# Kernel tuning notes

Hardware: AMD Instinct MI355X
Metric: run time of the kernel (lower is better)

Reference implementation:

```python
import jax, jax.numpy as jnp
import numpy as np

DIM = 2048          # SDR dimension
CTX = 512           # top-down context (grid code) dimension
B = 8192            # batch of independent samples
N_PV = DIM // 4     # 512 PV interneurons
N_SV = DIM // 8     # 256 SOM/VIP interneurons
ALPHA_POS = 1.0 / 10.0   # dt / tau_pos
ALPHA_NEG = 1.0 / 10.0   # dt / tau_neg


def setup_inputs() -> dict:
    key = jax.random.key(0)
    ks = jax.random.split(key, 14)
    sc = 1.0 / np.sqrt(DIM)
    sc_sv = 1.0 / np.sqrt(N_SV)
    xav = np.sqrt(6.0 / (CTX + DIM))  # xavier uniform bound for predictor
    u = lambda k, shp, s: jax.random.uniform(k, shp, dtype=jnp.float32) * s
    return {
        "x_batch": jax.random.uniform(ks[0], (B, DIM), dtype=jnp.float32),
        "context_batch": jax.random.normal(ks[1], (B, CTX), dtype=jnp.float32),
        "r_pos_batch": jax.random.uniform(ks[2], (B, DIM), dtype=jnp.float32),
        "r_neg_batch": jax.random.uniform(ks[3], (B, DIM), dtype=jnp.float32),
        "W_pred": jax.random.uniform(ks[4], (DIM, CTX), jnp.float32, -xav, xav),
        "b_pred": jnp.zeros((DIM,), jnp.float32),
        "W_pv1_ff": u(ks[5], (N_PV, DIM), sc),
        "W_pv2_td": u(ks[6], (N_PV, DIM), sc),
        "W_vip_td": u(ks[7], (N_SV, DIM), sc),
        "W_som_in": u(ks[8], (N_SV, DIM), sc),
        "W_vip_som": u(ks[9], (N_SV, N_SV), sc_sv),
        "W_inh_pe_pos": u(ks[10], (DIM, N_PV), sc),
        "W_inh_pe_neg": u(ks[11], (DIM, N_PV), sc),
        "W_som_dend": u(ks[12], (DIM, N_SV), sc),
    }


def reference(x_batch, context_batch, r_pos_batch, r_neg_batch,
              W_pred, b_pred, W_pv1_ff, W_pv2_td, W_vip_td, W_som_in,
              W_vip_som, W_inh_pe_pos, W_inh_pe_neg, W_som_dend):
    relu = jax.nn.relu
    # top-down prediction: (B, CTX) @ (CTX, DIM) -> (B, DIM)
    predicted = context_batch @ W_pred.T + b_pred
    # interneuron circuit (Nemati 2025)
    r_pv1 = relu(x_batch @ W_pv1_ff.T)                               # (B, N_PV)
    r_pv2 = relu(predicted @ W_pv2_td.T)                             # (B, N_PV)
    r_vip = relu(predicted @ W_vip_td.T)                             # (B, N_SV)
    r_som = relu(relu(x_batch @ W_som_in.T) - r_vip @ W_vip_som.T)   # (B, N_SV)
    # signed prediction errors with somatic/dendritic inhibition
    pe_pos = relu(x_batch - predicted - r_pv2 @ W_inh_pe_pos.T)
    pe_neg = relu(predicted - x_batch - r_pv1 @ W_inh_pe_neg.T - r_som @ W_som_dend.T)
    # low-pass temporal filter of PE states
    new_r_pos = (1.0 - ALPHA_POS) * r_pos_batch + ALPHA_POS * pe_pos
    new_r_neg = (1.0 - ALPHA_NEG) * r_neg_batch + ALPHA_NEG * pe_neg
    return (new_r_pos, new_r_neg)
```

## Files before the change

kernel.cpp:

```cpp
#include <hip/hip_runtime.h>
#include <hip/hip_bf16.h>
#include <stdint.h>
#include <stddef.h>

#define DIMV 2048
#define CTXV 512
#define BV   8192
#define NPV  512
#define NSV  256

typedef __attribute__((ext_vector_type(8))) __bf16 bf16x8;
typedef __attribute__((ext_vector_type(4))) __bf16 bf16x4;
typedef __attribute__((ext_vector_type(4))) float f32x4;

__device__ __forceinline__ size_t fmq(int base_r, int Cb, int lhi, int llo, int nks) {
    const int kc = (Cb >> 3) + (lhi >> 1);
    return ((size_t)(base_r >> 4) * nks + (kc >> 2)) * 64 + (size_t)(kc & 3) * 16 + llo;
}

struct FmJob { const float* src; char* dst; int lognks; int ld; int trans; };
struct FmArgs { FmJob j[12]; unsigned cum[13]; };

__global__ __launch_bounds__(256) void cvt_fm(FmArgs a) {
    const unsigned total = a.cum[12];
    for (unsigned c = blockIdx.x * blockDim.x + threadIdx.x; c < total;
         c += gridDim.x * blockDim.x) {
        int seg = 0;
#pragma unroll
        for (int t = 1; t < 12; ++t) seg = (c >= a.cum[t]) ? t : seg;
        const FmJob jb = a.j[seg];
        const unsigned q = c - a.cum[seg];
        const int llo = q & 15, ch = (q >> 4) & 3;
        const unsigned blk = q >> 6;
        const unsigned s = blk & ((1u << jb.lognks) - 1u);
        const unsigned g = blk >> jb.lognks;
        const int row = g * 16 + llo;
        const int k0  = s * 32 + ch * 8;
        bf16x8 o;
        if (!jb.trans) {
            f32x4 v0 = *(const f32x4*)(jb.src + (size_t)row * jb.ld + k0);
            f32x4 v1 = *(const f32x4*)(jb.src + (size_t)row * jb.ld + k0 + 4);
#pragma unroll
            for (int e = 0; e < 4; ++e) { o[e] = (__bf16)v0[e]; o[e + 4] = (__bf16)v1[e]; }
        } else {
#pragma unroll
            for (int e = 0; e < 8; ++e)
                o[e] = (__bf16)jb.src[(size_t)(k0 + e) * jb.ld + row];
        }
        *(bf16x8*)(jb.dst + (size_t)q * 16) = o;
    }
}

__global__ __launch_bounds__(512)
void bias_comb(const float* __restrict__ Wpv2, const float* __restrict__ Wvip,
               const float* __restrict__ b, float* __restrict__ out) {
    const int tid  = threadIdx.x;
    const int gw   = blockIdx.x * 8 + (tid >> 6);
    const int lane = tid & 63;
    const float* row = (gw < 512) ? (Wpv2 + (size_t)gw * 2048)
                                  : (Wvip + (size_t)(gw - 512) * 2048);
    float acc = 0.f;
#pragma unroll
    for (int c = 0; c < 8; ++c) {
        const int j = lane * 32 + c * 4;
        f32x4 w  = *(const f32x4*)(row + j);
        f32x4 bb = *(const f32x4*)(b + j);
#pragma unroll
        for (int e = 0; e < 4; ++e) acc += w[e] * bb[e];
    }
#pragma unroll
    for (int off = 32; off > 0; off >>= 1) acc += __shfl_down(acc, off);
    if (lane == 0) out[gw] = acc;
}

#define GEOM4                                                     \
    const int tid  = threadIdx.x;                                 \
    const int wave = tid >> 6;                                    \
    const int lane = tid & 63;                                    \
    const int lhi  = lane >> 4;                                   \
    const int llo  = lane & 15;                                   \
    const int wr   = wave >> 1;                                   \
    const int wc   = wave & 1;

#define SETPA(Abase, nksA_)                                                   \
    _Pragma("unroll")                                                         \
    for (int i_ = 0; i_ < 2; ++i_) {                                          \
        const int g_ = (m0 + wr * 32 + i_ * 16) >> 4;                         \
        pa[i_] = (const char*)(Abase) + ((size_t)g_ * (nksA_)) * 1024 + lane * 16; \
    }
#define SETPW(Wbase, nksW_, nbase)                                            \
    _Pragma("unroll")                                                         \
    for (int j_ = 0; j_ < 4; ++j_) {                                          \
        const int g_ = ((nbase) + wc * 64 + j_ * 16) >> 4;                    \
        pw[j_] = (const char*)(Wbase) + ((size_t)g_ * (nksW_)) * 1024 + lane * 16; \
    }
#define LD6(AF, BF, OFS)                                                      \
    _Pragma("unroll")                                                         \
    for (int i_ = 0; i_ < 2; ++i_) AF[i_] = *(const bf16x8*)(pa[i_] + (OFS)); \
    _Pragma("unroll")                                                         \
    for (int j_ = 0; j_ < 4; ++j_) BF[j_] = *(const bf16x8*)(pw[j_] + (OFS));
#define ADV2                                                                  \
    _Pragma("unroll")                                                         \
    for (int i_ = 0; i_ < 2; ++i_) pa[i_] += 2048;                            \
    _Pragma("unroll")                                                         \
    for (int j_ = 0; j_ < 4; ++j_) pw[j_] += 2048;
#define MFMA8(af, bfr, acc)                                                   \
    __builtin_amdgcn_s_setprio(1);                                            \
    _Pragma("unroll")                                                         \
    for (int i = 0; i < 2; ++i)                                               \
        _Pragma("unroll")                                                     \
        for (int j = 0; j < 4; ++j)                                           \
            acc[i][j] = __builtin_amdgcn_mfma_f32_16x16x32_bf16(bfr[j], af[i], acc[i][j], 0, 0, 0); \
    __builtin_amdgcn_s_setprio(0);

struct GemmDesc {
    const char* A; int nksA;
    const char* W1; const char* W2; int nksW;
    int NB1, ntN, nsteps, epi;
    const float* bias;
    const char* subp; int nksSub;
    char* out1; int nksO1; char* out2; int nksO2;
};

__global__ __launch_bounds__(256, 3)
void pe_gemm7(GemmDesc dA_, GemmDesc dB_, GemmDesc dC_, int s1, int s2)
{
    const int nwg = gridDim.x;
    const int bid = blockIdx.x;
    int wg = (bid & 7) * (nwg >> 3) + (bid >> 3);
    GemmDesc d = dA_;
    if (wg >= s2)      { d = dC_; wg -= s2; }
    else if (wg >= s1) { d = dB_; wg -= s1; }
    if (d.out1 == nullptr) return;

    const int bx = wg / d.ntN;
    const int by = wg - bx * d.ntN;
    const int m0 = bx * 64;
    const int n0 = by * 128;

    const bool reg2  = (d.W2 != nullptr) && (n0 >= d.NB1);
    const char* Wc   = reg2 ? d.W2 : d.W1;
    const int n0r    = reg2 ? (n0 - d.NB1) : n0;

    GEOM4

    const f32x4 fzero = {0.f, 0.f, 0.f, 0.f};
    f32x4 acc[2][4];
#pragma unroll
    for (int i = 0; i < 2; ++i)
#pragma unroll
        for (int j = 0; j < 4; ++j) acc[i][j] = fzero;

    const char* pa[2]; const char* pw[4];
    SETPA(d.A, d.nksA)
    SETPW(Wc, d.nksW, n0r)

    bf16x8 A0[2], B0[4], A1[2], B1[4];
    LD6(A0, B0, 0)
    const int half = d.nsteps >> 1;
    for (int it = 0; it < half; ++it) {
        LD6(A1, B1, 1024)
        MFMA8(A0, B0, acc)
        ADV2
        if (it + 1 < half) { LD6(A0, B0, 0) }
        MFMA8(A1, B1, acc)
    }

#pragma unroll
    for (int i = 0; i < 2; ++i) {
#pragma unroll
        for (int j = 0; j < 4; ++j) {
            const int base_r = m0 + wr * 32 + i * 16;
            const int CbL    = (reg2 ? n0r : n0) + wc * 64 + j * 16;
            if (d.epi == 0) {
                const int colg = n0 + wc * 64 + j * 16 + lhi * 4;
                f32x4 b4 = *(const f32x4*)(d.bias + colg);
                bf16x4 o;
#pragma unroll
                for (int r = 0; r < 4; ++r) o[r] = (__bf16)(acc[i][j][r] + b4[r]);
                *(bf16x4*)(d.out1 + fmq(base_r, CbL, lhi, llo, d.nksO1) * 16 + (lhi & 1) * 8) = o;
            } else if (d.epi == 1) {
                char* op     = reg2 ? d.out2 : d.out1;
                const int nk = reg2 ? d.nksO2 : d.nksO1;
                bf16x4 o;
#pragma unroll
                for (int r = 0; r < 4; ++r) o[r] = (__bf16)fmaxf(acc[i][j][r], 0.f);
                *(bf16x4*)(op + fmq(base_r, CbL, lhi, llo, nk) * 16 + (lhi & 1) * 8) = o;
            } else if (d.epi == 2) {
                bf16x4 s4 = *(const bf16x4*)(d.subp + fmq(base_r, CbL, lhi, llo, d.nksSub) * 16 + (lhi & 1) * 8);
                bf16x4 o;
#pragma unroll
                for (int r = 0; r < 4; ++r)
                    o[r] = (__bf16)fmaxf((float)s4[r] - acc[i][j][r], 0.f);
                *(bf16x4*)(d.out1 + fmq(base_r, CbL, lhi, llo, d.nksO1) * 16 + (lhi & 1) * 8) = o;
            } else if (d.epi == 3) {
                bf16x4 o;
#pragma unroll
                for (int r = 0; r < 4; ++r) o[r] = (__bf16)acc[i][j][r];
                *(bf16x4*)(d.out1 + fmq(base_r, CbL, lhi, llo, d.nksO1) * 16 + (lhi & 1) * 8) = o;
            } else {
                const int colg = n0 + wc * 64 + j * 16 + lhi * 4;
                f32x4 b4 = *(const f32x4*)(d.bias + colg);
                char* op     = reg2 ? d.out2 : d.out1;
                const int nk = reg2 ? d.nksO2 : d.nksO1;
                bf16x4 o;
#pragma unroll
                for (int r = 0; r < 4; ++r)
                    o[r] = (__bf16)fmaxf(acc[i][j][r] + b4[r], 0.f);
                *(bf16x4*)(op + fmq(base_r, CbL, lhi, llo, nk) * 16 + (lhi & 1) * 8) = o;
            }
        }
    }
}

__global__ __launch_bounds__(256, 3)
void pe_filt7(const char* __restrict__ rpv2f, const char* __restrict__ Wposf,
              const char* __restrict__ rpv1f, const char* __restrict__ rsomf,
              const char* __restrict__ Wneg1f, const char* __restrict__ Wneg2f,
              const char* __restrict__ xfm, const char* __restrict__ predfm,
              const float* __restrict__ rpos, const float* __restrict__ rneg,
              float* __restrict__ outp, float* __restrict__ outn)
{
    const int nwg = gridDim.x;
    const int bid = blockIdx.x;
    const int wg  = (bid & 7) * (nwg >> 3) + (bid >> 3);
    const int bx  = wg >> 4;
    const int by  = wg & 15;
    const int m0  = bx * 64;
    const int n0  = by * 128;

    GEOM4

    const f32x4 fzero = {0.f, 0.f, 0.f, 0.f};
    f32x4 acc[2][4];
#pragma unroll
    for (int i = 0; i < 2; ++i)
#pragma unroll
        for (int j = 0; j < 4; ++j) acc[i][j] = fzero;

    const char* pa[2]; const char* pw[4];
    bf16x8 A0[2], B0[4], A1[2], B1[4];

    SETPA(rpv2f, 16)
    SETPW(Wposf, 16, n0)
    LD6(A0, B0, 0)
    for (int it = 0; it < 8; ++it) {
        LD6(A1, B1, 1024)
        MFMA8(A0, B0, acc)
        ADV2
        if (it + 1 < 8) { LD6(A0, B0, 0) }
        MFMA8(A1, B1, acc)
    }
    SETPA(rpv1f, 16)
    SETPW(Wneg1f, 16, n0)
    LD6(A0, B0, 0)

#pragma unroll
    for (int i = 0; i < 2; ++i) {
#pragma unroll
        for (int j = 0; j < 4; ++j) {
            const int base_r = m0 + wr * 32 + i * 16;
            const int Cb     = n0 + wc * 64 + j * 16;
            const int rowg   = base_r + llo;
            const int colg   = Cb + lhi * 4;
            const size_t idx = (size_t)rowg * 2048 + colg;
            const size_t qx  = fmq(base_r, Cb, lhi, llo, 64) * 16 + (lhi & 1) * 8;
            f32x4 rp  = *(const f32x4*)(rpos + idx);
            bf16x4 xb = *(const bf16x4*)(xfm + qx);
            bf16x4 pb = *(const bf16x4*)(predfm + qx);
            f32x4 o;
#pragma unroll
            for (int r = 0; r < 4; ++r) {
                const float dd = (float)xb[r] - (float)pb[r];
                o[r] = 0.9f * rp[r] + 0.1f * fmaxf(dd - acc[i][j][r], 0.f);
            }
            *(f32x4*)(outp + idx) = o;
            acc[i][j] = fzero;
        }
    }

    for (int it = 0; it < 8; ++it) {
        LD6(A1, B1, 1024)
        MFMA8(A0, B0, acc)
        ADV2
        if (it + 1 < 8) { LD6(A0, B0, 0) }
        MFMA8(A1, B1, acc)
    }
    SETPA(rsomf, 8)
    SETPW(Wneg2f, 8, n0)
    LD6(A0, B0, 0)
    for (int it = 0; it < 4; ++it) {
        LD6(A1, B1, 1024)
        MFMA8(A0, B0, acc)
        ADV2
        if (it + 1 < 4) { LD6(A0, B0, 0) }
        MFMA8(A1, B1, acc)
    }

#pragma unroll
    for (int i = 0; i < 2; ++i) {
#pragma unroll
        for (int j = 0; j < 4; ++j) {
            const int base_r = m0 + wr * 32 + i * 16;
            const int Cb     = n0 + wc * 64 + j * 16;
            const int rowg   = base_r + llo;
            const int colg   = Cb + lhi * 4;
            const size_t idx = (size_t)rowg * 2048 + colg;
            const size_t qx  = fmq(base_r, Cb, lhi, llo, 64) * 16 + (lhi & 1) * 8;
            f32x4 rn  = *(const f32x4*)(rneg + idx);
            bf16x4 xb = *(const bf16x4*)(xfm + qx);
            bf16x4 pb = *(const bf16x4*)(predfm + qx);
            f32x4 o;
#pragma unroll
            for (int r = 0; r < 4; ++r) {
                const float dd = (float)pb[r] - (float)xb[r];
                o[r] = 0.9f * rn[r] + 0.1f * fmaxf(dd - acc[i][j][r], 0.f);
            }
            *(f32x4*)(outn + idx) = o;
        }
    }
}

extern "C" void kernel_launch(void* const* d_in, const int* in_sizes, int n_in,
                              void* d_out, int out_size, void* d_ws, size_t ws_size,
                              hipStream_t stream) {
    (void)in_sizes; (void)n_in; (void)out_size; (void)ws_size;

    const float* x       = (const float*)d_in[0];
    const float* ctx     = (const float*)d_in[1];
    const float* r_pos   = (const float*)d_in[2];
    const float* r_neg   = (const float*)d_in[3];
    const float* Wpred   = (const float*)d_in[4];
    const float* bpred   = (const float*)d_in[5];
    const float* Wpv1    = (const float*)d_in[6];
    const float* Wpv2    = (const float*)d_in[7];
    const float* Wvip    = (const float*)d_in[8];
    const float* Wsomin  = (const float*)d_in[9];
    const float* Wvipsom = (const float*)d_in[10];
    const float* Wpepos  = (const float*)d_in[11];
    const float* Wpeneg  = (const float*)d_in[12];
    const float* Wsomd   = (const float*)d_in[13];

    char* ws = (char*)d_ws;
    char* ctx_fm     = ws; ws += (size_t)BV * CTXV * 2;
    char* x_fm       = ws; ws += (size_t)BV * DIMV * 2;
    char* pred_fm    = ws; ws += (size_t)BV * DIMV * 2;
    char* rpv1_fm    = ws; ws += (size_t)BV * NPV * 2;
    char* rpv2_fm    = ws; ws += (size_t)BV * NPV * 2;
    char* rvip_fm    = ws; ws += (size_t)BV * NSV * 2;
    char* ssom_fm    = ws; ws += (size_t)BV * NSV * 2;
    char* rsom_fm    = ws; ws += (size_t)BV * NSV * 2;
    char* Wpred_fm   = ws; ws += (size_t)DIMV * CTXV * 2;
    char* WpredT_fm  = ws; ws += (size_t)CTXV * DIMV * 2;
    char* Wpv1_fm    = ws; ws += (size_t)NPV * DIMV * 2;
    char* Wpv2_fm    = ws; ws += (size_t)NPV * DIMV * 2;
    char* Wvip_fm    = ws; ws += (size_t)NSV * DIMV * 2;
    char* Wsomin_fm  = ws; ws += (size_t)NSV * DIMV * 2;
    char* Wvipsom_fm = ws; ws += (size_t)NSV * NSV * 2;
    char* Wpepos_fm  = ws; ws += (size_t)DIMV * NPV * 2;
    char* Wpeneg_fm  = ws; ws += (size_t)DIMV * NPV * 2;
    char* Wsomd_fm   = ws; ws += (size_t)DIMV * NSV * 2;
    char* Wcomb2_fm  = ws; ws += (size_t)NPV * CTXV * 2;
    char* Wcombv_fm  = ws; ws += (size_t)NSV * CTXV * 2;
    float* biascomb  = (float*)ws; ws += 768 * 4;

    float* out_pos = (float*)d_out;
    float* out_neg = out_pos + (size_t)BV * DIMV;

    FmArgs fa;
    auto setj = [&](int t, const float* s, char* dst, int lognks, int ld, int trans) {
        fa.j[t].src = s; fa.j[t].dst = dst; fa.j[t].lognks = lognks;
        fa.j[t].ld = ld; fa.j[t].trans = trans;
    };
    setj(0,  ctx,     ctx_fm,     4, 512,  0);
    setj(1,  x,       x_fm,       6, 2048, 0);
    setj(2,  Wpred,   Wpred_fm,   4, 512,  0);
    setj(3,  Wpred,   WpredT_fm,  6, 512,  1);
    setj(4,  Wpv1,    Wpv1_fm,    6, 2048, 0);
    setj(5,  Wpv2,    Wpv2_fm,    6, 2048, 0);
    setj(6,  Wvip,    Wvip_fm,    6, 2048, 0);
    setj(7,  Wsomin,  Wsomin_fm,  6, 2048, 0);
    setj(8,  Wvipsom, Wvipsom_fm, 3, 256,  0);
    setj(9,  Wpepos,  Wpepos_fm,  4, 512,  0);
    setj(10, Wpeneg,  Wpeneg_fm,  4, 512,  0);
    setj(11, Wsomd,   Wsomd_fm,   3, 256,  0);
    const unsigned cum[13] = {0u, 524288u, 2621440u, 2752512u, 2883584u,
                              3014656u, 3145728u, 3211264u, 3276800u,
                              3284992u, 3416064u, 3547136u, 3612672u};
    for (int t = 0; t < 13; ++t) fa.cum[t] = cum[t];
    cvt_fm<<<dim3(2048), dim3(256), 0, stream>>>(fa);
    bias_comb<<<dim3(96), dim3(512), 0, stream>>>(Wpv2, Wvip, bpred, biascomb);

    const int BIG = 1 << 28;
    GemmDesc dz;
    dz.A = nullptr; dz.nksA = 1; dz.W1 = dz.W2 = nullptr; dz.nksW = 1;
    dz.NB1 = BIG; dz.ntN = 1; dz.nsteps = 2; dz.epi = 3;
    dz.bias = nullptr; dz.subp = nullptr; dz.nksSub = 1;
    dz.out1 = nullptr; dz.nksO1 = 1; dz.out2 = nullptr; dz.nksO2 = 1;

    GemmDesc d_pred = dz;
    d_pred.A = ctx_fm; d_pred.nksA = 16;
    d_pred.W1 = Wpred_fm; d_pred.nksW = 16;
    d_pred.ntN = 16; d_pred.nsteps = 16; d_pred.epi = 0;
    d_pred.bias = bpred; d_pred.out1 = pred_fm; d_pred.nksO1 = 64;

    GemmDesc d_c2 = dz;
    d_c2.A = Wpv2_fm; d_c2.nksA = 64;
    d_c2.W1 = WpredT_fm; d_c2.nksW = 64;
    d_c2.ntN = 4; d_c2.nsteps = 64; d_c2.epi = 3;
    d_c2.out1 = Wcomb2_fm; d_c2.nksO1 = 16;

    GemmDesc d_cv = d_c2;
    d_cv.A = Wvip_fm;
    d_cv.out1 = Wcombv_fm; d_cv.nksO1 = 16;

    pe_gemm7<<<dim3(2096), dim3(256), 0, stream>>>(d_pred, d_c2, d_cv, 2048, 2080);

    GemmDesc d_23 = dz;
    d_23.A = x_fm; d_23.nksA = 64;
    d_23.W1 = Wpv1_fm; d_23.W2 = Wsomin_fm; d_23.nksW = 64;
    d_23.NB1 = NPV; d_23.ntN = 6; d_23.nsteps = 64; d_23.epi = 1;
    d_23.out1 = rpv1_fm; d_23.nksO1 = 16;
    d_23.out2 = ssom_fm; d_23.nksO2 = 8;

    GemmDesc d_45 = dz;
    d_45.A = ctx_fm; d_45.nksA = 16;
    d_45.W1 = Wcomb2_fm; d_45.W2 = Wcombv_fm; d_45.nksW = 16;
    d_45.NB1 = NPV; d_45.ntN = 6; d_45.nsteps = 16; d_45.epi = 4;
    d_45.bias = biascomb;
    d_45.out1 = rpv2_fm; d_45.nksO1 = 16;
    d_45.out2 = rvip_fm; d_45.nksO2 = 8;

    pe_gemm7<<<dim3(1536), dim3(256), 0, stream>>>(d_23, d_45, dz, 768, 1536);

    GemmDesc d_som = dz;
    d_som.A = rvip_fm; d_som.nksA = 8;
    d_som.W1 = Wvipsom_fm; d_som.nksW = 8;
    d_som.ntN = 2; d_som.nsteps = 8; d_som.epi = 2;
    d_som.subp = ssom_fm; d_som.nksSub = 8;
    d_som.out1 = rsom_fm; d_som.nksO1 = 8;

    pe_gemm7<<<dim3(256), dim3(256), 0, stream>>>(d_som, d_som, d_som, 256, 512);

    pe_filt7<<<dim3(2048), dim3(256), 0, stream>>>(
        rpv2_fm, Wpepos_fm, rpv1_fm, rsom_fm, Wpeneg_fm, Wsomd_fm,
        x_fm, pred_fm, r_pos, r_neg, out_pos, out_neg);
}
```

Measured before the change: 321.2 us.

## Fuse x minus prediction into the prediction GEMM epilogue and use 512-thread tiles

The prediction GEMM epilogue now reads x and writes the difference x - pred into a single bf16 buffer. The filter kernel then loads one array instead of both x and pred in each of its positive and negative passes, which cuts global traffic. All GEMM and filter kernels also move to 512-thread blocks with 128-row M tiles, halving the grid sizes. The larger blocks with a min-blocks hint of 3 may squeeze the register budget, and bf16 rounding now applies to the difference instead of to pred alone.

```diff
diff --git a/kernel.cpp b/kernel.cpp
--- a/kernel.cpp
+++ b/kernel.cpp
@@ -73,13 +73,13 @@
     if (lane == 0) out[gw] = acc;
 }
 
-#define GEOM4                                                     \
+#define GEOM8                                                     \
     const int tid  = threadIdx.x;                                 \
     const int wave = tid >> 6;                                    \
     const int lane = tid & 63;                                    \
     const int lhi  = lane >> 4;                                   \
     const int llo  = lane & 15;                                   \
-    const int wr   = wave >> 1;                                   \
+    const int wr   = wave >> 1;                         \
     const int wc   = wave & 1;
 
 #define SETPA(Abase, nksA_)                                                   \
@@ -122,8 +122,8 @@
     char* out1; int nksO1; char* out2; int nksO2;
 };
 
-__global__ __launch_bounds__(256, 3)
-void pe_gemm7(GemmDesc dA_, GemmDesc dB_, GemmDesc dC_, int s1, int s2)
+__global__ __launch_bounds__(512, 3)
+void pe_gemm9(GemmDesc dA_, GemmDesc dB_, GemmDesc dC_, int s1, int s2)
 {
     const int nwg = gridDim.x;
     const int bid = blockIdx.x;
@@ -135,14 +135,14 @@
 
     const int bx = wg / d.ntN;
     const int by = wg - bx * d.ntN;
-    const int m0 = bx * 64;
+    const int m0 = bx * 128;
     const int n0 = by * 128;
 
     const bool reg2  = (d.W2 != nullptr) && (n0 >= d.NB1);
     const char* Wc   = reg2 ? d.W2 : d.W1;
     const int n0r    = reg2 ? (n0 - d.NB1) : n0;
 
-    GEOM4
+    GEOM8
 
     const f32x4 fzero = {0.f, 0.f, 0.f, 0.f};
     f32x4 acc[2][4];
@@ -175,9 +175,11 @@
             if (d.epi == 0) {
                 const int colg = n0 + wc * 64 + j * 16 + lhi * 4;
                 f32x4 b4 = *(const f32x4*)(d.bias + colg);
+                bf16x4 xb = *(const bf16x4*)(d.subp + fmq(base_r, CbL, lhi, llo, d.nksSub) * 16 + (lhi & 1) * 8);
                 bf16x4 o;
 #pragma unroll
-                for (int r = 0; r < 4; ++r) o[r] = (__bf16)(acc[i][j][r] + b4[r]);
+                for (int r = 0; r < 4; ++r)
+                    o[r] = (__bf16)((float)xb[r] - (acc[i][j][r] + b4[r]));
                 *(bf16x4*)(d.out1 + fmq(base_r, CbL, lhi, llo, d.nksO1) * 16 + (lhi & 1) * 8) = o;
             } else if (d.epi == 1) {
                 char* op     = reg2 ? d.out2 : d.out1;
@@ -213,11 +215,11 @@
     }
 }
 
-__global__ __launch_bounds__(256, 3)
-void pe_filt7(const char* __restrict__ rpv2f, const char* __restrict__ Wposf,
+__global__ __launch_bounds__(512, 3)
+void pe_filt9(const char* __restrict__ rpv2f, const char* __restrict__ Wposf,
               const char* __restrict__ rpv1f, const char* __restrict__ rsomf,
               const char* __restrict__ Wneg1f, const char* __restrict__ Wneg2f,
-              const char* __restrict__ xfm, const char* __restrict__ predfm,
+              const char* __restrict__ difff,
               const float* __restrict__ rpos, const float* __restrict__ rneg,
               float* __restrict__ outp, float* __restrict__ outn)
 {
@@ -226,10 +228,10 @@
     const int wg  = (bid & 7) * (nwg >> 3) + (bid >> 3);
     const int bx  = wg >> 4;
     const int by  = wg & 15;
-    const int m0  = bx * 64;
+    const int m0  = bx * 128;
     const int n0  = by * 128;
 
-    GEOM4
+    GEOM8
 
     const f32x4 fzero = {0.f, 0.f, 0.f, 0.f};
     f32x4 acc[2][4];
@@ -266,14 +268,11 @@
             const size_t idx = (size_t)rowg * 2048 + colg;
             const size_t qx  = fmq(base_r, Cb, lhi, llo, 64) * 16 + (lhi & 1) * 8;
             f32x4 rp  = *(const f32x4*)(rpos + idx);
-            bf16x4 xb = *(const bf16x4*)(xfm + qx);
-            bf16x4 pb = *(const bf16x4*)(predfm + qx);
+            bf16x4 db = *(const bf16x4*)(difff + qx);
             f32x4 o;
 #pragma unroll
-            for (int r = 0; r < 4; ++r) {
-                const float dd = (float)xb[r] - (float)pb[r];
-                o[r] = 0.9f * rp[r] + 0.1f * fmaxf(dd - acc[i][j][r], 0.f);
-            }
+            for (int r = 0; r < 4; ++r)
+                o[r] = 0.9f * rp[r] + 0.1f * fmaxf((float)db[r] - acc[i][j][r], 0.f);
             *(f32x4*)(outp + idx) = o;
             acc[i][j] = fzero;
         }
@@ -308,14 +307,11 @@
             const size_t idx = (size_t)rowg * 2048 + colg;
             const size_t qx  = fmq(base_r, Cb, lhi, llo, 64) * 16 + (lhi & 1) * 8;
             f32x4 rn  = *(const f32x4*)(rneg + idx);
-            bf16x4 xb = *(const bf16x4*)(xfm + qx);
-            bf16x4 pb = *(const bf16x4*)(predfm + qx);
+            bf16x4 db = *(const bf16x4*)(difff + qx);
             f32x4 o;
 #pragma unroll
-            for (int r = 0; r < 4; ++r) {
-                const float dd = (float)pb[r] - (float)xb[r];
-                o[r] = 0.9f * rn[r] + 0.1f * fmaxf(dd - acc[i][j][r], 0.f);
-            }
+            for (int r = 0; r < 4; ++r)
+                o[r] = 0.9f * rn[r] + 0.1f * fmaxf(-(float)db[r] - acc[i][j][r], 0.f);
             *(f32x4*)(outn + idx) = o;
         }
     }
@@ -344,7 +340,7 @@
     char* ws = (char*)d_ws;
     char* ctx_fm     = ws; ws += (size_t)BV * CTXV * 2;
     char* x_fm       = ws; ws += (size_t)BV * DIMV * 2;
-    char* pred_fm    = ws; ws += (size_t)BV * DIMV * 2;
+    char* diff_fm    = ws; ws += (size_t)BV * DIMV * 2;
     char* rpv1_fm    = ws; ws += (size_t)BV * NPV * 2;
     char* rpv2_fm    = ws; ws += (size_t)BV * NPV * 2;
     char* rvip_fm    = ws; ws += (size_t)BV * NSV * 2;
@@ -402,7 +398,9 @@
     d_pred.A = ctx_fm; d_pred.nksA = 16;
     d_pred.W1 = Wpred_fm; d_pred.nksW = 16;
     d_pred.ntN = 16; d_pred.nsteps = 16; d_pred.epi = 0;
-    d_pred.bias = bpred; d_pred.out1 = pred_fm; d_pred.nksO1 = 64;
+    d_pred.bias = bpred;
+    d_pred.subp = x_fm; d_pred.nksSub = 64;
+    d_pred.out1 = diff_fm; d_pred.nksO1 = 64;
 
     GemmDesc d_c2 = dz;
     d_c2.A = Wpv2_fm; d_c2.nksA = 64;
@@ -414,7 +412,7 @@
     d_cv.A = Wvip_fm;
     d_cv.out1 = Wcombv_fm; d_cv.nksO1 = 16;
 
-    pe_gemm7<<<dim3(2096), dim3(256), 0, stream>>>(d_pred, d_c2, d_cv, 2048, 2080);
+    pe_gemm9<<<dim3(1048), dim3(512), 0, stream>>>(d_pred, d_c2, d_cv, 1024, 1040);
 
     GemmDesc d_23 = dz;
     d_23.A = x_fm; d_23.nksA = 64;
@@ -431,7 +429,7 @@
     d_45.out1 = rpv2_fm; d_45.nksO1 = 16;
     d_45.out2 = rvip_fm; d_45.nksO2 = 8;
 
-    pe_gemm7<<<dim3(1536), dim3(256), 0, stream>>>(d_23, d_45, dz, 768, 1536);
+    pe_gemm9<<<dim3(768), dim3(512), 0, stream>>>(d_23, d_45, dz, 384, 768);
 
     GemmDesc d_som = dz;
     d_som.A = rvip_fm; d_som.nksA = 8;
@@ -440,9 +438,9 @@
     d_som.subp = ssom_fm; d_som.nksSub = 8;
     d_som.out1 = rsom_fm; d_som.nksO1 = 8;
 
-    pe_gemm7<<<dim3(256), dim3(256), 0, stream>>>(d_som, d_som, d_som, 256, 512);
-
-    pe_filt7<<<dim3(2048), dim3(256), 0, stream>>>(
+    pe_gemm9<<<dim3(128), dim3(512), 0, stream>>>(d_som, d_som, d_som, 128, 128);
+
+    pe_filt9<<<dim3(1024), dim3(512), 0, stream>>>(
         rpv2_fm, Wpepos_fm, rpv1_fm, rsom_fm, Wpeneg_fm, Wsomd_fm,
-        x_fm, pred_fm, r_pos, r_neg, out_pos, out_neg);
-}
+        diff_fm, r_pos, r_neg, out_pos, out_neg);
+}
```

After: 337.9 us. 5.2% more time.
